# Optimization experiments

Hardware: AMD Instinct MI355X
Metric: run time of the kernel (lower is better)

Reference implementation:

```python
import jax, jax.numpy as jnp
import numpy as np

LN_EPS = 1e-5

def _layernorm(x, g, b):
    mu = jnp.mean(x, axis=-1, keepdims=True)
    var = jnp.mean(jnp.square(x - mu), axis=-1, keepdims=True)
    return (x - mu) * jax.lax.rsqrt(var + LN_EPS) * g + b

def setup_inputs() -> dict:
    key = jax.random.key(0)
    ks = jax.random.split(key, 8)
    B, T, C = 4, 2048, 1024
    s = 0.02
    return {
        "x": jax.random.normal(ks[0], (B, T, C), jnp.float32),
        "w_qkv": jax.random.normal(ks[1], (C, 3 * C), jnp.float32) * s,
        "b_qkv": jnp.zeros((3 * C,), jnp.float32),
        "w_out": jax.random.normal(ks[2], (C, C), jnp.float32) * s,
        "b_out": jnp.zeros((C,), jnp.float32),
        "w1": jax.random.normal(ks[3], (C, 4 * C), jnp.float32) * s,
        "b1": jnp.zeros((4 * C,), jnp.float32),
        "w2": jax.random.normal(ks[4], (4 * C, C), jnp.float32) * s,
        "b2": jnp.zeros((C,), jnp.float32),
        "g1": jnp.ones((C,), jnp.float32),
        "be1": jnp.zeros((C,), jnp.float32),
        "g2": jnp.ones((C,), jnp.float32),
        "be2": jnp.zeros((C,), jnp.float32),
        "n_head": 16,
    }

def reference(x, w_qkv, b_qkv, w_out, b_out, w1, b1, w2, b2, g1, be1, g2, be2, n_head):
    B, T, C = x.shape
    H = n_head
    D = C // H
    # --- causal self-attention ---
    qkv = x @ w_qkv + b_qkv                      # [B,T,3C]
    q, k, v = jnp.split(qkv, 3, axis=-1)
    q = q.reshape(B, T, H, D).transpose(0, 2, 1, 3)  # [B,H,T,D]
    k = k.reshape(B, T, H, D).transpose(0, 2, 1, 3)
    v = v.reshape(B, T, H, D).transpose(0, 2, 1, 3)
    attn = jnp.einsum("bhqd,bhkd->bhqk", q, k) * (1.0 / np.sqrt(D))
    causal = jnp.tril(jnp.ones((T, T), bool))
    attn = jnp.where(causal, attn, jnp.float32(-jnp.inf))
    attn = jax.nn.softmax(attn, axis=-1)
    y = jnp.einsum("bhqk,bhkd->bhqd", attn, v)
    y = y.transpose(0, 2, 1, 3).reshape(B, T, C)
    y = y @ w_out + b_out
    # post-norm residual (norm applied to sublayer output)
    x = x + _layernorm(y, g1, be1)
    # --- MLP ---
    h = jax.nn.gelu(x @ w1 + b1, approximate=False)
    h = h @ w2 + b2
    x = x + _layernorm(h, g2, be2)
    return x
```

## Files before the change

### kernel.cpp

```cpp
#include <hip/hip_runtime.h>
#include <hip/hip_bf16.h>

typedef unsigned short ushort_t;
using bf16x8 = __attribute__((ext_vector_type(8))) short;
using f32x4  = __attribute__((ext_vector_type(4))) float;

#define DEV __device__ __forceinline__

DEV unsigned short f2bf(float f) {
    unsigned int u = __builtin_bit_cast(unsigned int, f);
    u = (u + 0x7fffu + ((u >> 16) & 1u)) >> 16;
    return (unsigned short)u;
}

DEV int cvtpk_bf16(float lo, float hi) {
    int r;
    asm("v_cvt_pk_bf16_f32 %0, %1, %2" : "=v"(r) : "v"(lo), "v"(hi));
    return r;
}

DEV void gload16(const unsigned short* g, unsigned short* l) {
    __builtin_amdgcn_global_load_lds(
        (const __attribute__((address_space(1))) void*)g,
        (__attribute__((address_space(3))) void*)l, 16, 0, 0);
}

DEV float gelu_f(float v) {
    float u = v * (0.79788456f + 0.03567741f * v * v);
    float t = __builtin_amdgcn_exp2f(u * 2.88539008f);
    return v * t * __builtin_amdgcn_rcpf(t + 1.0f);
}

__global__ __launch_bounds__(256) void cvtbf_kernel(const float* __restrict__ in,
                                                    unsigned short* __restrict__ out) {
    int i = (blockIdx.x * 256 + threadIdx.x) * 4;
    float4 v = *(const float4*)&in[i];
    out[i + 0] = f2bf(v.x);
    out[i + 1] = f2bf(v.y);
    out[i + 2] = f2bf(v.z);
    out[i + 3] = f2bf(v.w);
}

__global__ __launch_bounds__(256) void transpose_cvt_kernel(const float* __restrict__ in,
                                                            unsigned short* __restrict__ out,
                                                            int R, int C) {
    __shared__ float t[32][33];
    int tx = threadIdx.x, ty = threadIdx.y;
    int c0 = blockIdx.x * 32, r0 = blockIdx.y * 32;
#pragma unroll
    for (int i = 0; i < 4; ++i)
        t[ty + i * 8][tx] = in[(size_t)(r0 + ty + i * 8) * C + c0 + tx];
    __syncthreads();
#pragma unroll
    for (int i = 0; i < 4; ++i)
        out[(size_t)(c0 + ty + i * 8) * R + r0 + tx] = f2bf(t[tx][ty + i * 8]);
}

__global__ __launch_bounds__(256) void vtrans_kernel(const unsigned short* __restrict__ qkvb,
                                                     unsigned short* __restrict__ vtg) {
    __shared__ unsigned short t[64 * 66];
    const int tid = threadIdx.x;
    const int t0 = blockIdx.x * 64;
    const int bh = blockIdx.y;
    const int b = bh >> 4, h = bh & 15;
    const unsigned short* src = qkvb + (size_t)(b * 2048 + t0) * 3072 + 2048 + h * 64;
#pragma unroll
    for (int c = 0; c < 2; ++c) {
        int cid = c * 256 + tid;
        int row = cid >> 3, cc = cid & 7;
        *(int4*)&t[row * 66 + cc * 8] = *(const int4*)&src[(size_t)row * 3072 + cc * 8];
    }
    __syncthreads();
    unsigned short* dst = vtg + (size_t)bh * 64 * 2048 + t0;
#pragma unroll
    for (int c = 0; c < 2; ++c) {
        int cid = c * 256 + tid;
        int d = cid >> 3, cc2 = cid & 7;
        bf16x8 v;
#pragma unroll
        for (int j = 0; j < 8; ++j) v[j] = (short)t[(cc2 * 8 + j) * 66 + d];
        *(bf16x8*)&dst[(size_t)d * 2048 + cc2 * 8] = v;
    }
}

template <int BM, int ACT, int OBF>
__global__ __launch_bounds__(512, 2) void gemm256_kernel(
    const unsigned short* __restrict__ A, const unsigned short* __restrict__ Bt,
    const float* __restrict__ bias, void* __restrict__ out,
    int N, int K, int gridNt) {
    constexpr int MF = BM / 32;
    constexpr int MH = MF / 2;
    constexpr int ACH = BM * 8;
    constexpr int ALD = BM / 64;
    constexpr int LB = (BM == 256) ? 8 : 7;
    __shared__ __align__(16) unsigned short lA[2][ACH * 8];
    __shared__ __align__(16) unsigned short lB[2][2048 * 8];
    const int tid = threadIdx.x;
    const int lane = tid & 63, wid = tid >> 6;
    const int g = lane >> 4, lr = lane & 15;
    const int wm = wid >> 2, wn = wid & 3;

    const int nwg = gridDim.x, cpx = nwg >> 3, bid = blockIdx.x;
    const int wkid = (bid & 7) * cpx + (bid >> 3);
    const int mt = wkid / gridNt, nt = wkid % gridNt;
    const int m0 = mt * BM, n0 = nt * 256;

    auto stageA = [&](int s, int kt, int bb) {
        int c = s * 512 + tid;
        int row = c & (BM - 1), kb = c >> LB;
        gload16(&A[(size_t)(m0 + row) * K + kt * 64 + kb * 8],
                &lA[bb][(size_t)(s * 512 + (tid & ~63)) * 8]);
    };
    auto stageB = [&](int s, int kt, int bb) {
        int c = s * 512 + tid;
        int row = c & 255, kb = c >> 8;
        gload16(&Bt[(size_t)(n0 + row) * K + kt * 64 + kb * 8],
                &lB[bb][(size_t)(s * 512 + (tid & ~63)) * 8]);
    };

    f32x4 acc[MF][4] = {};
    bf16x8 af[MH];
    bf16x8 bfr[4];

    const int nkt = K >> 6;
    if constexpr (BM == 256) {
        stageA(0, 0, 0); stageA(1, 0, 0); stageB(0, 0, 0); stageB(1, 0, 0);
        stageA(2, 0, 0); stageA(3, 0, 0); stageB(2, 0, 0); stageB(3, 0, 0);
    } else {
        stageA(0, 0, 0); stageB(0, 0, 0); stageB(1, 0, 0);
        stageA(1, 0, 0); stageB(2, 0, 0); stageB(3, 0, 0);
    }

    for (int kt = 0; kt < nkt; ++kt) {
        const int b = kt & 1;
        const int ktn = kt + 1;
        const bool more = (ktn < nkt);
#pragma unroll
        for (int p = 0; p < 4; ++p) {
            const int ks = p >> 1, mh = p & 1;
            if (p == 0) {
                if constexpr (BM == 256) asm volatile("s_waitcnt vmcnt(4)" ::: "memory");
                else                     asm volatile("s_waitcnt vmcnt(3)" ::: "memory");
                __builtin_amdgcn_s_barrier();
                __builtin_amdgcn_sched_barrier(0);
            } else if (p == 2) {
                if (more) {
                    if constexpr (BM == 256) asm volatile("s_waitcnt vmcnt(4)" ::: "memory");
                    else                     asm volatile("s_waitcnt vmcnt(3)" ::: "memory");
                } else {
                    asm volatile("s_waitcnt vmcnt(0)" ::: "memory");
                }
                __builtin_amdgcn_s_barrier();
                __builtin_amdgcn_sched_barrier(0);
            }
#pragma unroll
            for (int mf2 = 0; mf2 < MH; ++mf2) {
                int row = wm * (BM / 2) + (mh * MH + mf2) * 16 + lr;
                int c = (ks * 4 + g) * BM + row;
                af[mf2] = *(const bf16x8*)&lA[b][(size_t)c * 8];
            }
            if (mh == 0) {
#pragma unroll
                for (int nf = 0; nf < 4; ++nf) {
                    int row = wn * 64 + nf * 16 + lr;
                    int c = (ks * 4 + g) * 256 + row;
                    bfr[nf] = *(const bf16x8*)&lB[b][(size_t)c * 8];
                }
            }
            if (more) {
                if constexpr (BM == 256) {
                    if (p == 0) { stageA(0, ktn, b ^ 1); stageA(1, ktn, b ^ 1); }
                    else if (p == 1) { stageB(0, ktn, b ^ 1); stageB(1, ktn, b ^ 1); }
                    else if (p == 2) { stageA(2, ktn, b ^ 1); stageA(3, ktn, b ^ 1); }
                    else { stageB(2, ktn, b ^ 1); stageB(3, ktn, b ^ 1); }
                } else {
                    if (p == 0) { stageA(0, ktn, b ^ 1); stageB(0, ktn, b ^ 1); }
                    else if (p == 1) { stageB(1, ktn, b ^ 1); }
                    else if (p == 2) { stageA(1, ktn, b ^ 1); stageB(2, ktn, b ^ 1); }
                    else { stageB(3, ktn, b ^ 1); }
                }
            }
            __builtin_amdgcn_sched_barrier(0);
            __builtin_amdgcn_s_barrier();
            asm volatile("s_waitcnt lgkmcnt(0)" ::: "memory");
            __builtin_amdgcn_sched_barrier(0);
            __builtin_amdgcn_s_setprio(1);
#pragma unroll
            for (int mf2 = 0; mf2 < MH; ++mf2)
#pragma unroll
                for (int nf = 0; nf < 4; ++nf) {
                    int mf = mh * MH + mf2;
                    acc[mf][nf] = __builtin_amdgcn_mfma_f32_16x16x32_bf16(
                        af[mf2], bfr[nf], acc[mf][nf], 0, 0, 0);
                }
            __builtin_amdgcn_s_setprio(0);
            __builtin_amdgcn_sched_barrier(0);
        }
    }

#pragma unroll
    for (int mf = 0; mf < MF; ++mf) {
#pragma unroll
        for (int nf = 0; nf < 4; ++nf) {
            int col = n0 + wn * 64 + nf * 16 + lr;
            float bv = bias[col];
#pragma unroll
            for (int r = 0; r < 4; ++r) {
                int row = m0 + wm * (BM / 2) + mf * 16 + g * 4 + r;
                float v = acc[mf][nf][r] + bv;
                if (ACT == 1) v = gelu_f(v);
                if (OBF)
                    ((unsigned short*)out)[(size_t)row * N + col] = f2bf(v);
                else
                    ((float*)out)[(size_t)row * N + col] = v;
            }
        }
    }
}

__global__ __launch_bounds__(256) void attn_kernel(const unsigned short* __restrict__ qkv,
                                                   const unsigned short* __restrict__ vtg,
                                                   unsigned short* __restrict__ y) {
    __shared__ unsigned short Kl[2][4096];
    __shared__ unsigned short Vl[2][4096];
    const int tid = threadIdx.x, lane = tid & 63, w = tid >> 6;
    const int g = lane >> 4, lr = lane & 15;
    const int p = blockIdx.x, h = blockIdx.y, b = blockIdx.z;
    const int bh = b * 16 + h;
    const size_t rs3 = 3072;
    const unsigned short* qbase = qkv + (size_t)b * 2048 * rs3 + h * 64;
    const unsigned short* kbase = qbase + 1024;
    const unsigned short* vbase = vtg + (size_t)bh * 64 * 2048;

    int ksoff[2], vsoff[2], ldoff[2];
#pragma unroll
    for (int c = 0; c < 2; ++c) {
        int row = w * 16 + c * 8 + (lane >> 3);
        int ccs = (lane & 7) ^ (row & 7) ^ (row >> 3);
        ksoff[c] = row * 3072 + ccs * 8;
        vsoff[c] = row * 2048 + ccs * 8;
        ldoff[c] = (w * 16 + c * 8) * 64;
    }

    const int idxP0 = 4 * (32 * (g & 1) + lr);
    const int idxP1 = idxP0 + 64;
    int idxA[4];
#pragma unroll
    for (int r = 0; r < 4; ++r) idxA[r] = 4 * (g * 20 + r);
    const bool ghigh = (g >> 1) != 0;
    const float qscale = 0.125f * 1.44269504089f;

    auto process = [&](int J) {
        const int q0w = J * 128 + w * 32;
        const int ktend = 2 * J + 2;
#pragma unroll
        for (int c = 0; c < 2; ++c) {
            gload16(&kbase[ksoff[c]], &Kl[0][ldoff[c]]);
            gload16(&vbase[vsoff[c]], &Vl[0][ldoff[c]]);
        }
        int qf[2][2][4];
#pragma unroll
        for (int sub = 0; sub < 2; ++sub)
#pragma unroll
            for (int f = 0; f < 2; ++f) {
                int4 v = *(const int4*)&qbase[(size_t)(q0w + sub * 16 + lr) * rs3 + f * 32 + g * 8];
                int vv[4] = {v.x, v.y, v.z, v.w};
#pragma unroll
                for (int i = 0; i < 4; ++i) {
                    unsigned int u = (unsigned int)vv[i];
                    float lo = __builtin_bit_cast(float, u << 16) * qscale;
                    float hi = __builtin_bit_cast(float, u & 0xffff0000u) * qscale;
                    qf[sub][f][i] = cvtpk_bf16(lo, hi);
                }
            }

        f32x4 O[2][4] = {};
        float m_[2] = {-3.0e38f, -3.0e38f}, l_[2] = {0.f, 0.f};

        int buf = 0;
        for (int kt = 0; kt < ktend; ++kt) {
            asm volatile("s_waitcnt vmcnt(0)" ::: "memory");
            __builtin_amdgcn_s_barrier();
            __builtin_amdgcn_sched_barrier(0);
            if (kt + 1 < ktend) {
#pragma unroll
                for (int c = 0; c < 2; ++c) {
                    gload16(&kbase[(size_t)(kt + 1) * 64 * 3072 + ksoff[c]], &Kl[buf ^ 1][ldoff[c]]);
                    gload16(&vbase[vsoff[c] + (kt + 1) * 64], &Vl[buf ^ 1][ldoff[c]]);
                }
            }
            const unsigned short* Kc = Kl[buf];
            const unsigned short* Vc = Vl[buf];

            const bool act0 = (kt * 64) <= (q0w + 15);
            const bool act1 = (kt * 64) <= (q0w + 31);

            f32x4 s0[4], s1[4];
#pragma unroll
            for (int st = 0; st < 4; ++st) {
                int rbase = (st * 16 + lr) * 64;
                int sw = (lr & 7) ^ (st * 2 + (lr >> 3));
                bf16x8 kf0 = *(const bf16x8*)&Kc[rbase + ((g ^ sw) * 8)];
                bf16x8 kf1 = *(const bf16x8*)&Kc[rbase + (((4 + g) ^ sw) * 8)];
                if (act0) {
                    f32x4 a = {};
                    a = __builtin_amdgcn_mfma_f32_16x16x32_bf16(kf0, *(const bf16x8*)&qf[0][0], a, 0, 0, 0);
                    a = __builtin_amdgcn_mfma_f32_16x16x32_bf16(kf1, *(const bf16x8*)&qf[0][1], a, 0, 0, 0);
                    s0[st] = a;
                }
                if (act1) {
                    f32x4 a = {};
                    a = __builtin_amdgcn_mfma_f32_16x16x32_bf16(kf0, *(const bf16x8*)&qf[1][0], a, 0, 0, 0);
                    a = __builtin_amdgcn_mfma_f32_16x16x32_bf16(kf1, *(const bf16x8*)&qf[1][1], a, 0, 0, 0);
                    s1[st] = a;
                }
            }

            int wt0[2][4], wt1[2][4];
#pragma unroll
            for (int sub = 0; sub < 2; ++sub) {
                if (sub == 0 && !act0) continue;
                if (sub == 1 && !act1) continue;
                f32x4* s = (sub == 0) ? s0 : s1;
                const int qmin = q0w + sub * 16;
                if (kt * 64 + 63 > qmin) {
                    int qv = qmin + lr;
#pragma unroll
                    for (int st = 0; st < 4; ++st) {
                        int keyb = kt * 64 + st * 16 + g * 4;
#pragma unroll
                        for (int r = 0; r < 4; ++r)
                            if (keyb + r > qv) s[st][r] = -3.0e38f;
                    }
                }
                float mx = fmaxf(fmaxf(s[0][0], s[0][1]), fmaxf(s[0][2], s[0][3]));
#pragma unroll
                for (int st = 1; st < 4; ++st)
                    mx = fmaxf(mx, fmaxf(fmaxf(s[st][0], s[st][1]), fmaxf(s[st][2], s[st][3])));
                mx = fmaxf(mx, __shfl_xor(mx, 16));
                mx = fmaxf(mx, __shfl_xor(mx, 32));
                float mold = m_[sub];
                float mnew = fmaxf(mold, mx);
                float alpha = __builtin_amdgcn_exp2f(mold - mnew);
                m_[sub] = mnew;
                float rs = 0.f;
#pragma unroll
                for (int st = 0; st < 4; ++st)
#pragma unroll
                    for (int r = 0; r < 4; ++r) {
                        float pp = __builtin_amdgcn_exp2f(s[st][r] - mnew);
                        s[st][r] = pp;
                        rs += pp;
                    }
                rs += __shfl_xor(rs, 16);
                rs += __shfl_xor(rs, 32);
                l_[sub] = l_[sub] * alpha + rs;
                int av = __builtin_bit_cast(int, alpha);
                f32x4* Os = O[sub];
#pragma unroll
                for (int r = 0; r < 4; ++r) {
                    float ar = __builtin_bit_cast(float, __builtin_amdgcn_ds_bpermute(idxA[r], av));
#pragma unroll
                    for (int dt = 0; dt < 4; ++dt) Os[dt][r] *= ar;
                }
                int ws_[4][2];
#pragma unroll
                for (int st = 0; st < 4; ++st) {
                    ws_[st][0] = cvtpk_bf16(s[st][0], s[st][1]);
                    ws_[st][1] = cvtpk_bf16(s[st][2], s[st][3]);
                }
                int(*wt)[4] = (sub == 0) ? wt0 : wt1;
#pragma unroll
                for (int ks = 0; ks < 2; ++ks)
#pragma unroll
                    for (int hp = 0; hp < 4; ++hp) {
                        int idx = (hp < 2) ? idxP0 : idxP1;
                        int v0 = __builtin_amdgcn_ds_bpermute(idx, ws_[2 * ks][hp & 1]);
                        int v1 = __builtin_amdgcn_ds_bpermute(idx, ws_[2 * ks + 1][hp & 1]);
                        wt[ks][hp] = ghigh ? v1 : v0;
                    }
            }

#pragma unroll
            for (int ks = 0; ks < 2; ++ks) {
                bf16x8 pa0 = *(const bf16x8*)&wt0[ks][0];
                bf16x8 pa1 = *(const bf16x8*)&wt1[ks][0];
#pragma unroll
                for (int dt = 0; dt < 4; ++dt) {
                    int d = dt * 16 + lr;
                    int xv = (ks * 4 + g) ^ (lr & 7) ^ (dt * 2 + (lr >> 3));
                    bf16x8 vf = *(const bf16x8*)&Vc[d * 64 + xv * 8];
                    if (act0) O[0][dt] = __builtin_amdgcn_mfma_f32_16x16x32_bf16(pa0, vf, O[0][dt], 0, 0, 0);
                    if (act1) O[1][dt] = __builtin_amdgcn_mfma_f32_16x16x32_bf16(pa1, vf, O[1][dt], 0, 0, 0);
                }
            }
            buf ^= 1;
        }

#pragma unroll
        for (int sub = 0; sub < 2; ++sub) {
            int lv = __builtin_bit_cast(int, l_[sub]);
#pragma unroll
            for (int r = 0; r < 4; ++r) {
                float lval = __builtin_bit_cast(float, __builtin_amdgcn_ds_bpermute(idxA[r], lv));
                float inv = __builtin_amdgcn_rcpf(lval);
                int q = q0w + sub * 16 + g * 4 + r;
#pragma unroll
                for (int dt = 0; dt < 4; ++dt)
                    y[(size_t)(b * 2048 + q) * 1024 + h * 64 + dt * 16 + lr] =
                        f2bf(O[sub][dt][r] * inv);
            }
        }
    };

    process(15 - p);
    __syncthreads();
    process(p);
}

template <int WRITE_BF>
__global__ __launch_bounds__(256) void ln_kernel(const float* __restrict__ base,
                                                 const float* __restrict__ delta,
                                                 const float* __restrict__ gw,
                                                 const float* __restrict__ bw,
                                                 float* __restrict__ outf,
                                                 unsigned short* __restrict__ outb) {
    const int row = blockIdx.x;
    const int tid = threadIdx.x;
    const float* d = delta + (size_t)row * 1024;
    const float* bs = base + (size_t)row * 1024;
    float4 x = *(const float4*)&d[tid * 4];
    float s = x.x + x.y + x.z + x.w;
    float s2 = x.x * x.x + x.y * x.y + x.z * x.z + x.w * x.w;
#pragma unroll
    for (int off = 1; off < 64; off <<= 1) {
        s += __shfl_xor(s, off);
        s2 += __shfl_xor(s2, off);
    }
    __shared__ float red[8];
    if ((tid & 63) == 0) {
        red[tid >> 6] = s;
        red[4 + (tid >> 6)] = s2;
    }
    __syncthreads();
    s = red[0] + red[1] + red[2] + red[3];
    s2 = red[4] + red[5] + red[6] + red[7];
    float mu = s * (1.f / 1024.f);
    float var = s2 * (1.f / 1024.f) - mu * mu;
    float rsig = rsqrtf(var + 1e-5f);
    float4 bb = *(const float4*)&bs[tid * 4];
    float4 gv = *(const float4*)&gw[tid * 4];
    float4 bv = *(const float4*)&bw[tid * 4];
    float4 o;
    o.x = bb.x + (x.x - mu) * rsig * gv.x + bv.x;
    o.y = bb.y + (x.y - mu) * rsig * gv.y + bv.y;
    o.z = bb.z + (x.z - mu) * rsig * gv.z + bv.z;
    o.w = bb.w + (x.w - mu) * rsig * gv.w + bv.w;
    *(float4*)&outf[(size_t)row * 1024 + tid * 4] = o;
    if (WRITE_BF) {
        unsigned short* ob = outb + (size_t)row * 1024 + tid * 4;
        ob[0] = f2bf(o.x);
        ob[1] = f2bf(o.y);
        ob[2] = f2bf(o.z);
        ob[3] = f2bf(o.w);
    }
}

extern "C" void kernel_launch(void* const* d_in, const int* in_sizes, int n_in,
                              void* d_out, int out_size, void* d_ws, size_t ws_size,
                              hipStream_t stream) {
    const float* x = (const float*)d_in[0];
    const float* w_qkv = (const float*)d_in[1];
    const float* b_qkv = (const float*)d_in[2];
    const float* w_out = (const float*)d_in[3];
    const float* b_out = (const float*)d_in[4];
    const float* w1 = (const float*)d_in[5];
    const float* b1 = (const float*)d_in[6];
    const float* w2 = (const float*)d_in[7];
    const float* b2 = (const float*)d_in[8];
    const float* g1 = (const float*)d_in[9];
    const float* be1 = (const float*)d_in[10];
    const float* g2 = (const float*)d_in[11];
    const float* be2 = (const float*)d_in[12];

    const size_t MB = 1ull << 20;
    if (ws_size < 184 * MB) return;
    char* ws = (char*)d_ws;
    unsigned short* xb    = (unsigned short*)(ws + 0);
    unsigned short* vtg   = (unsigned short*)(ws + 0);
    unsigned short* wqkvt = (unsigned short*)(ws + 16 * MB);
    unsigned short* qkvb  = (unsigned short*)(ws + 22 * MB);
    unsigned short* hb    = (unsigned short*)(ws + 0);
    unsigned short* woutt = (unsigned short*)(ws + 70 * MB);
    unsigned short* yb    = (unsigned short*)(ws + 72 * MB);
    float*          attnp = (float*)(ws + 88 * MB);
    float*          ff    = (float*)(ws + 88 * MB);
    float*          x2f   = (float*)(ws + 120 * MB);
    unsigned short* x2b   = (unsigned short*)(ws + 152 * MB);
    unsigned short* w1t   = (unsigned short*)(ws + 168 * MB);
    unsigned short* w2t   = (unsigned short*)(ws + 176 * MB);

    cvtbf_kernel<<<8192, 256, 0, stream>>>(x, xb);
    transpose_cvt_kernel<<<dim3(96, 32), dim3(32, 8), 0, stream>>>(w_qkv, wqkvt, 1024, 3072);
    transpose_cvt_kernel<<<dim3(32, 32), dim3(32, 8), 0, stream>>>(w_out, woutt, 1024, 1024);
    transpose_cvt_kernel<<<dim3(128, 32), dim3(32, 8), 0, stream>>>(w1, w1t, 1024, 4096);
    transpose_cvt_kernel<<<dim3(32, 128), dim3(32, 8), 0, stream>>>(w2, w2t, 4096, 1024);
    gemm256_kernel<256, 0, 1><<<384, 512, 0, stream>>>(xb, wqkvt, b_qkv, qkvb, 3072, 1024, 12);
    vtrans_kernel<<<dim3(32, 64), 256, 0, stream>>>(qkvb, vtg);
    attn_kernel<<<dim3(8, 16, 4), 256, 0, stream>>>(qkvb, vtg, yb);
    gemm256_kernel<128, 0, 0><<<256, 512, 0, stream>>>(yb, woutt, b_out, attnp, 1024, 1024, 4);
    ln_kernel<1><<<8192, 256, 0, stream>>>(x, attnp, g1, be1, x2f, x2b);
    gemm256_kernel<256, 1, 1><<<512, 512, 0, stream>>>(x2b, w1t, b1, hb, 4096, 1024, 16);
    gemm256_kernel<128, 0, 0><<<256, 512, 0, stream>>>(hb, w2t, b2, ff, 1024, 4096, 4);
    ln_kernel<0><<<8192, 256, 0, stream>>>(x2f, ff, g2, be2, (float*)d_out, nullptr);
}
```

Measured before the change: 538.3 us.

## Restructure GEMM main loop into two k-substeps with fewer barriers

The GEMM inner loop used four phases per 64-wide k-tile. Each phase had its own barriers, an explicit LDS wait and scheduling fences. It now runs two k-substeps, each loading all A and B fragments and issuing the next half-tile's global-to-LDS copies. It drops the second barrier, the lgkmcnt wait and the sched_barrier fences so the compiler can interleave LDS reads with MFMAs; the attention loop also loses one sched_barrier. This cuts synchronization overhead but holds twice as many A fragments in registers, which may raise register pressure under the 2-blocks-per-CU launch bound.

```diff
diff --git a/kernel.cpp b/kernel.cpp
--- a/kernel.cpp
+++ b/kernel.cpp
@@ -89,12 +89,11 @@
     const float* __restrict__ bias, void* __restrict__ out,
     int N, int K, int gridNt) {
     constexpr int MF = BM / 32;
-    constexpr int MH = MF / 2;
-    constexpr int ACH = BM * 8;
     constexpr int ALD = BM / 64;
+    constexpr int NW = ALD / 2 + 2;
     constexpr int LB = (BM == 256) ? 8 : 7;
-    __shared__ __align__(16) unsigned short lA[2][ACH * 8];
-    __shared__ __align__(16) unsigned short lB[2][2048 * 8];
+    __shared__ __align__(16) unsigned short lA[2][BM * 64];
+    __shared__ __align__(16) unsigned short lB[2][256 * 64];
     const int tid = threadIdx.x;
     const int lane = tid & 63, wid = tid >> 6;
     const int g = lane >> 4, lr = lane & 15;
@@ -117,84 +116,59 @@
         gload16(&Bt[(size_t)(n0 + row) * K + kt * 64 + kb * 8],
                 &lB[bb][(size_t)(s * 512 + (tid & ~63)) * 8]);
     };
+    auto stageKh = [&](int half, int kt, int bb) {
+        if constexpr (BM == 256) {
+            stageA(half * 2 + 0, kt, bb);
+            stageA(half * 2 + 1, kt, bb);
+            stageB(half * 2 + 0, kt, bb);
+            stageB(half * 2 + 1, kt, bb);
+        } else {
+            stageA(half, kt, bb);
+            stageB(half * 2 + 0, kt, bb);
+            stageB(half * 2 + 1, kt, bb);
+        }
+    };
 
     f32x4 acc[MF][4] = {};
-    bf16x8 af[MH];
+    bf16x8 af[MF];
     bf16x8 bfr[4];
 
     const int nkt = K >> 6;
-    if constexpr (BM == 256) {
-        stageA(0, 0, 0); stageA(1, 0, 0); stageB(0, 0, 0); stageB(1, 0, 0);
-        stageA(2, 0, 0); stageA(3, 0, 0); stageB(2, 0, 0); stageB(3, 0, 0);
-    } else {
-        stageA(0, 0, 0); stageB(0, 0, 0); stageB(1, 0, 0);
-        stageA(1, 0, 0); stageB(2, 0, 0); stageB(3, 0, 0);
-    }
+    stageKh(0, 0, 0);
+    stageKh(1, 0, 0);
 
     for (int kt = 0; kt < nkt; ++kt) {
         const int b = kt & 1;
-        const int ktn = kt + 1;
-        const bool more = (ktn < nkt);
-#pragma unroll
-        for (int p = 0; p < 4; ++p) {
-            const int ks = p >> 1, mh = p & 1;
-            if (p == 0) {
-                if constexpr (BM == 256) asm volatile("s_waitcnt vmcnt(4)" ::: "memory");
-                else                     asm volatile("s_waitcnt vmcnt(3)" ::: "memory");
-                __builtin_amdgcn_s_barrier();
-                __builtin_amdgcn_sched_barrier(0);
-            } else if (p == 2) {
-                if (more) {
-                    if constexpr (BM == 256) asm volatile("s_waitcnt vmcnt(4)" ::: "memory");
-                    else                     asm volatile("s_waitcnt vmcnt(3)" ::: "memory");
-                } else {
-                    asm volatile("s_waitcnt vmcnt(0)" ::: "memory");
-                }
-                __builtin_amdgcn_s_barrier();
-                __builtin_amdgcn_sched_barrier(0);
-            }
-#pragma unroll
-            for (int mf2 = 0; mf2 < MH; ++mf2) {
-                int row = wm * (BM / 2) + (mh * MH + mf2) * 16 + lr;
-                int c = (ks * 4 + g) * BM + row;
-                af[mf2] = *(const bf16x8*)&lA[b][(size_t)c * 8];
-            }
-            if (mh == 0) {
-#pragma unroll
-                for (int nf = 0; nf < 4; ++nf) {
-                    int row = wn * 64 + nf * 16 + lr;
-                    int c = (ks * 4 + g) * 256 + row;
-                    bfr[nf] = *(const bf16x8*)&lB[b][(size_t)c * 8];
-                }
-            }
-            if (more) {
-                if constexpr (BM == 256) {
-                    if (p == 0) { stageA(0, ktn, b ^ 1); stageA(1, ktn, b ^ 1); }
-                    else if (p == 1) { stageB(0, ktn, b ^ 1); stageB(1, ktn, b ^ 1); }
-                    else if (p == 2) { stageA(2, ktn, b ^ 1); stageA(3, ktn, b ^ 1); }
-                    else { stageB(2, ktn, b ^ 1); stageB(3, ktn, b ^ 1); }
-                } else {
-                    if (p == 0) { stageA(0, ktn, b ^ 1); stageB(0, ktn, b ^ 1); }
-                    else if (p == 1) { stageB(1, ktn, b ^ 1); }
-                    else if (p == 2) { stageA(1, ktn, b ^ 1); stageB(2, ktn, b ^ 1); }
-                    else { stageB(3, ktn, b ^ 1); }
-                }
-            }
-            __builtin_amdgcn_sched_barrier(0);
+        const bool more = (kt + 1 < nkt);
+#pragma unroll
+        for (int ks = 0; ks < 2; ++ks) {
+            if (ks == 1 && !more)
+                asm volatile("s_waitcnt vmcnt(0)" ::: "memory");
+            else if constexpr (BM == 256)
+                asm volatile("s_waitcnt vmcnt(4)" ::: "memory");
+            else
+                asm volatile("s_waitcnt vmcnt(3)" ::: "memory");
             __builtin_amdgcn_s_barrier();
-            asm volatile("s_waitcnt lgkmcnt(0)" ::: "memory");
-            __builtin_amdgcn_sched_barrier(0);
+            asm volatile("" ::: "memory");
+#pragma unroll
+            for (int mf = 0; mf < MF; ++mf) {
+                int c = (ks * 4 + g) * BM + wm * (BM / 2) + mf * 16 + lr;
+                af[mf] = *(const bf16x8*)&lA[b][(size_t)c * 8];
+            }
+#pragma unroll
+            for (int nf = 0; nf < 4; ++nf) {
+                int c = (ks * 4 + g) * 256 + wn * 64 + nf * 16 + lr;
+                bfr[nf] = *(const bf16x8*)&lB[b][(size_t)c * 8];
+            }
+            if (more) stageKh(ks, kt + 1, b ^ 1);
             __builtin_amdgcn_s_setprio(1);
 #pragma unroll
-            for (int mf2 = 0; mf2 < MH; ++mf2)
-#pragma unroll
-                for (int nf = 0; nf < 4; ++nf) {
-                    int mf = mh * MH + mf2;
+            for (int mf = 0; mf < MF; ++mf)
+#pragma unroll
+                for (int nf = 0; nf < 4; ++nf)
                     acc[mf][nf] = __builtin_amdgcn_mfma_f32_16x16x32_bf16(
-                        af[mf2], bfr[nf], acc[mf][nf], 0, 0, 0);
-                }
+                        af[mf], bfr[nf], acc[mf][nf], 0, 0, 0);
             __builtin_amdgcn_s_setprio(0);
-            __builtin_amdgcn_sched_barrier(0);
         }
     }
 
@@ -281,7 +255,7 @@
         for (int kt = 0; kt < ktend; ++kt) {
             asm volatile("s_waitcnt vmcnt(0)" ::: "memory");
             __builtin_amdgcn_s_barrier();
-            __builtin_amdgcn_sched_barrier(0);
+            asm volatile("" ::: "memory");
             if (kt + 1 < ktend) {
 #pragma unroll
                 for (int c = 0; c < 2; ++c) {
```

Result: faster. 511.6 us (-5.0%).
